# Kernel tuning notes

Hardware: AMD Instinct MI355X
Metric: run time of the kernel (lower is better)

The kernel has to match this reference:

```python
import jax, jax.numpy as jnp
import numpy as np

N_SRC = 100000
N_EDGES = 1000000
IN_FEATS = 64
N_CLASSES = 64


def setup_inputs() -> dict:
    key = jax.random.key(0)
    k1, k2, k3, k4, k5 = jax.random.split(key, 5)
    x = jax.random.normal(k1, (N_SRC, IN_FEATS), dtype=jnp.float32)
    W_self = jax.random.normal(k2, (IN_FEATS, N_CLASSES), dtype=jnp.float32) / np.sqrt(IN_FEATS)
    W_neigh = jax.random.normal(k3, (IN_FEATS, N_CLASSES), dtype=jnp.float32) / np.sqrt(IN_FEATS)
    b = jnp.zeros((N_CLASSES,), dtype=jnp.float32)
    src = jax.random.randint(k4, (N_EDGES,), 0, N_SRC, dtype=jnp.int32)
    dst = jax.random.randint(k5, (N_EDGES,), 0, N_SRC, dtype=jnp.int32)
    return {"x": x, "W_self": W_self, "W_neigh": W_neigh, "b": b,
            "src": src, "dst": dst, "num_dst": N_SRC}


def reference(x, W_self, W_neigh, b, src, dst, num_dst):
    # SAGEConv 'mean': gather src features along edges, segment-mean into dst,
    # then rst = h_dst @ W_self + h_neigh_mean @ W_neigh + b, followed by relu.
    msgs = x[src]                                                   # [E, F] irregular gather
    summed = jax.ops.segment_sum(msgs, dst, num_segments=num_dst)   # [num_dst, F]
    deg = jax.ops.segment_sum(jnp.ones((src.shape[0],), x.dtype), dst,
                              num_segments=num_dst)                 # [num_dst]
    h_neigh = summed / jnp.maximum(deg, 1.0)[:, None]               # mean (0 for isolated)
    h_dst = x[:num_dst]
    h = h_dst @ W_self + h_neigh @ W_neigh + b
    return jax.nn.relu(h)
```

## Files before the change

### kernel.cpp

```cpp
#include <hip/hip_runtime.h>


constexpr int F = 64;
constexpr int BROWS = 256;
constexpr int MAXNB = 512;
constexpr int CHP = 4096;
constexpr int LCAP = 4096;
constexpr int LDK = 136;

typedef __attribute__((ext_vector_type(8))) short short8;
typedef __attribute__((ext_vector_type(4))) float float4v;

__device__ inline unsigned short f2bf(float f) {
    union { float f; unsigned u; } c; c.f = f;
    unsigned u = c.u;
    return (unsigned short)((u + 0x7FFFu + ((u >> 16) & 1u)) >> 16);
}
__device__ inline float bf2f(unsigned short h) {
    union { unsigned u; float f; } c; c.u = (unsigned)h << 16;
    return c.f;
}

__global__ __launch_bounds__(256) void k_conv(const float* __restrict__ x,
                                              const float* __restrict__ Ws,
                                              const float* __restrict__ Wn,
                                              unsigned short* __restrict__ xb,
                                              unsigned short* __restrict__ WtG,
                                              const int* __restrict__ dst,
                                              int* __restrict__ cnt,
                                              long n4, int n_edges, int nchunk) {
    __shared__ int hist[MAXNB];
    int t = threadIdx.x;
    long tid = (long)blockIdx.x * 256 + t;
    if (tid < 2 * F * F) {
        int i = (int)tid;
        int n = i & 63, k = i >> 6;
        float v = (k < 64) ? Ws[k * 64 + n] : Wn[(k - 64) * 64 + n];
        WtG[n * 128 + k] = f2bf(v);
    }
    int c = blockIdx.x;
    if (c < nchunk) {
        for (int i = t; i < MAXNB; i += 256) hist[i] = 0;
        __syncthreads();
        int e0 = c * CHP, e1 = min(e0 + CHP, n_edges);
        for (int e = e0 + t; e < e1; e += 256) atomicAdd(&hist[dst[e] >> 8], 1);
        __syncthreads();
        for (int i = t; i < MAXNB; i += 256) cnt[(long)c * MAXNB + i] = hist[i];
    }
    for (long i = tid; i < n4; i += (long)gridDim.x * 256) {
        float4 v = ((const float4*)x)[i];
        ushort4 o;
        o.x = f2bf(v.x); o.y = f2bf(v.y); o.z = f2bf(v.z); o.w = f2bf(v.w);
        ((ushort4*)xb)[i] = o;
    }
}

__global__ __launch_bounds__(512) void k_scanA(int* __restrict__ cnt,
                                               int* __restrict__ btot, int nchunk) {
    int b = (blockIdx.x * 512 + threadIdx.x) >> 6;
    int lane = threadIdx.x & 63;
    if (b >= MAXNB) return;
    int per = (nchunk + 63) / 64;
    int c0 = lane * per;
    int vals[16];
    int lsum = 0;
#pragma unroll
    for (int i = 0; i < 16; ++i) {
        if (i < per) {
            int c = c0 + i;
            int v = (c < nchunk) ? cnt[(long)c * MAXNB + b] : 0;
            vals[i] = v; lsum += v;
        }
    }
    int incl = lsum;
    for (int off = 1; off < 64; off <<= 1) {
        int o = __shfl_up(incl, off);
        if (lane >= off) incl += o;
    }
    int run = incl - lsum;
#pragma unroll
    for (int i = 0; i < 16; ++i) {
        if (i < per) {
            int c = c0 + i;
            if (c < nchunk) { cnt[(long)c * MAXNB + b] = run; run += vals[i]; }
        }
    }
    int tot = __shfl(incl, 63);
    if (lane == 0) btot[b] = tot;
}

__global__ __launch_bounds__(512) void k_scanB(const int* __restrict__ btot,
                                               int* __restrict__ bstart) {
    __shared__ int wtot[8];
    __shared__ int woff[8];
    int t = threadIdx.x;
    int lane = t & 63, wave = t >> 6;
    int v = btot[t];
    int incl = v;
    for (int off = 1; off < 64; off <<= 1) {
        int o = __shfl_up(incl, off);
        if (lane >= off) incl += o;
    }
    if (lane == 63) wtot[wave] = incl;
    __syncthreads();
    if (t == 0) { int s = 0; for (int i = 0; i < 8; ++i) { woff[i] = s; s += wtot[i]; } }
    __syncthreads();
    bstart[t] = incl - v + woff[wave];
    if (t == 511) bstart[MAXNB] = woff[7] + incl;
}

__global__ __launch_bounds__(512) void k_place(const int* __restrict__ src,
                                               const int* __restrict__ dst,
                                               const int* __restrict__ cnt,
                                               const int* __restrict__ bstart,
                                               unsigned* __restrict__ pay, int n_edges) {
    __shared__ int sbp[MAXNB];
    __shared__ int lstart[MAXNB];
    __shared__ int lcur[MAXNB];
    __shared__ unsigned spay[CHP];
    __shared__ int sgpos[CHP];
    __shared__ int wtot[8];
    __shared__ int woff[8];
    int t = threadIdx.x;
    int c = blockIdx.x;
    int e0 = c * CHP, e1 = min(e0 + CHP, n_edges);
    sbp[t] = bstart[t] + cnt[(long)c * MAXNB + t];
    lcur[t] = 0;
    __syncthreads();
    for (int e = e0 + t; e < e1; e += 512) atomicAdd(&lcur[dst[e] >> 8], 1);
    __syncthreads();
    int lane = t & 63, wave = t >> 6;
    int v = lcur[t];
    int incl = v;
    for (int off = 1; off < 64; off <<= 1) {
        int o = __shfl_up(incl, off);
        if (lane >= off) incl += o;
    }
    if (lane == 63) wtot[wave] = incl;
    __syncthreads();
    if (t == 0) { int s = 0; for (int i = 0; i < 8; ++i) { woff[i] = s; s += wtot[i]; } }
    __syncthreads();
    lstart[t] = incl - v + woff[wave];
    lcur[t] = 0;
    __syncthreads();
    for (int e = e0 + t; e < e1; e += 512) {
        int d = dst[e];
        int b = d >> 8;
        int rank = atomicAdd(&lcur[b], 1);
        int idx = lstart[b] + rank;
        spay[idx] = ((unsigned)src[e] << 8) | (unsigned)(d & 255);
        sgpos[idx] = sbp[b] + rank;
    }
    __syncthreads();
    int n = e1 - e0;
    for (int i = t; i < n; i += 512) pay[sgpos[i]] = spay[i];
}

__global__ __launch_bounds__(256) void k_agg(const unsigned short* __restrict__ xb,
                                             const unsigned* __restrict__ pay,
                                             const int* __restrict__ bstart,
                                             unsigned short* __restrict__ hb,
                                             int num_dst) {
    __shared__ int degs[64];
    __shared__ int rs[64];
    __shared__ int cur[64];
    __shared__ int scsr[LCAP];
    int t = threadIdx.x;
    int blk = blockIdx.x;
    int b = blk >> 2, q = blk & 3;
    int s0 = bstart[b], s1 = bstart[b + 1];
    if (t < 64) degs[t] = 0;
    __syncthreads();
    for (int i = s0 + t; i < s1; i += 256) {
        int row = pay[i] & 255;
        if ((row >> 6) == q) atomicAdd(&degs[row & 63], 1);
    }
    __syncthreads();
    if (t < 64) {
        int v = degs[t];
        int incl = v;
        for (int off = 1; off < 64; off <<= 1) {
            int o = __shfl_up(incl, off);
            if (t >= off) incl += o;
        }
        rs[t] = incl - v;
        cur[t] = incl - v;
    }
    __syncthreads();
    for (int i = s0 + t; i < s1; i += 256) {
        unsigned p = pay[i];
        int row = p & 255;
        if ((row >> 6) == q) {
            int pos = atomicAdd(&cur[row & 63], 1);
            if (pos < LCAP) scsr[pos] = (int)(p >> 8);
        }
    }
    __syncthreads();

    int lane = t & 63;
    int wave = t >> 6;
    int g = lane >> 3;
    int c8 = (lane & 7) * 8;
#pragma unroll
    for (int batch = 0; batch < 2; ++batch) {
        int rl = wave * 16 + batch * 8 + g;
        int grow = b * BROWS + q * 64 + rl;
        int deg = degs[rl];
        int base = rs[rl];
        float acc[8] = {0.f, 0.f, 0.f, 0.f, 0.f, 0.f, 0.f, 0.f};
        for (int k = 0; k < deg; k += 4) {
            int dm = deg - 1;
            int i0 = scsr[base + k];
            int i1 = scsr[base + min(k + 1, dm)];
            int i2 = scsr[base + min(k + 2, dm)];
            int i3 = scsr[base + min(k + 3, dm)];
            short8 u0 = *(const short8*)&xb[(long)i0 * F + c8];
            short8 u1 = *(const short8*)&xb[(long)i1 * F + c8];
            short8 u2 = *(const short8*)&xb[(long)i2 * F + c8];
            short8 u3 = *(const short8*)&xb[(long)i3 * F + c8];
#pragma unroll
            for (int j = 0; j < 8; ++j) acc[j] += bf2f((unsigned short)u0[j]);
            if (k + 1 < deg) {
#pragma unroll
                for (int j = 0; j < 8; ++j) acc[j] += bf2f((unsigned short)u1[j]);
            }
            if (k + 2 < deg) {
#pragma unroll
                for (int j = 0; j < 8; ++j) acc[j] += bf2f((unsigned short)u2[j]);
            }
            if (k + 3 < deg) {
#pragma unroll
                for (int j = 0; j < 8; ++j) acc[j] += bf2f((unsigned short)u3[j]);
            }
        }
        if (grow < num_dst) {
            float inv = 1.0f / fmaxf((float)deg, 1.0f);
            short8 o;
#pragma unroll
            for (int j = 0; j < 8; ++j) o[j] = (short)f2bf(acc[j] * inv);
            *(short8*)&hb[(long)grow * F + c8] = o;
        }
    }
}

__global__ __launch_bounds__(256) void k_gemm_mfma(
    const unsigned short* __restrict__ xb, const unsigned short* __restrict__ hb,
    const unsigned short* __restrict__ WtG,
    const float* __restrict__ b, float* __restrict__ out, int num_dst)
{
    __shared__ __align__(16) unsigned short Atile[64 * LDK];
    __shared__ __align__(16) unsigned short Wt[64 * LDK];
    int t = threadIdx.x;
    int row0 = blockIdx.x * 64;

    for (int i = t; i < 64 * 16; i += 256) {
        int r = i >> 4, s = i & 15;
        *(short8*)&Wt[r * LDK + s * 8] = *(const short8*)&WtG[r * 128 + s * 8];
        int g = row0 + r;
        short8 v = {0, 0, 0, 0, 0, 0, 0, 0};
        if (g < num_dst)
            v = (s < 8) ? *(const short8*)&xb[(long)g * F + s * 8]
                        : *(const short8*)&hb[(long)g * F + (s - 8) * 8];
        *(short8*)&Atile[r * LDK + s * 8] = v;
    }
    __syncthreads();

    int lane = t & 63;
    int wave = t >> 6;
    int m = lane & 15;
    int quad = lane >> 4;
    const unsigned short* arow = &Atile[(wave * 16 + m) * LDK + quad * 8];

    float4v acc[4];
#pragma unroll
    for (int nt = 0; nt < 4; ++nt) acc[nt] = (float4v){0.f, 0.f, 0.f, 0.f};

#pragma unroll
    for (int kb = 0; kb < 4; ++kb) {
        short8 a = *(const short8*)(arow + kb * 32);
#pragma unroll
        for (int nt = 0; nt < 4; ++nt) {
            short8 bf = *(const short8*)&Wt[(nt * 16 + m) * LDK + quad * 8 + kb * 32];
            acc[nt] = __builtin_amdgcn_mfma_f32_16x16x32_bf16(a, bf, acc[nt], 0, 0, 0);
        }
    }

    int gr_base = row0 + wave * 16 + quad * 4;
#pragma unroll
    for (int nt = 0; nt < 4; ++nt) {
        int col = nt * 16 + m;
        float bias = b[col];
#pragma unroll
        for (int rg = 0; rg < 4; ++rg) {
            int g = gr_base + rg;
            if (g < num_dst) out[(long)g * F + col] = fmaxf(acc[nt][rg] + bias, 0.0f);
        }
    }
}

__global__ __launch_bounds__(256) void k_scatter(const float* __restrict__ x, const int* __restrict__ src,
                                                 const int* __restrict__ dst, float* __restrict__ summed,
                                                 float* __restrict__ degf, int n_edges) {
    long tid = (long)blockIdx.x * 256 + threadIdx.x;
    int e = (int)(tid >> 6);
    if (e >= n_edges) return;
    int f = threadIdx.x & 63;
    atomicAdd(&summed[(long)dst[e] * F + f], x[(long)src[e] * F + f]);
    if (f == 0) atomicAdd(&degf[dst[e]], 1.0f);
}

__global__ __launch_bounds__(256) void k_gemm_shfl(
    const float* __restrict__ x, const float* __restrict__ Ws, const float* __restrict__ Wn,
    const float* __restrict__ b, const float* __restrict__ degf, float* inout, int num_dst)
{
    __shared__ float Wl[2 * F * F];
    for (int i = threadIdx.x; i < F * F; i += 256) { Wl[i] = Ws[i]; Wl[F * F + i] = Wn[i]; }
    __syncthreads();
    int lane = threadIdx.x & 63;
    int r = (blockIdx.x * 256 + threadIdx.x) >> 6;
    if (r >= num_dst) return;
    float xv = x[(long)r * F + lane];
    float hv = inout[(long)r * F + lane] / fmaxf(degf[r], 1.0f);
    float acc = b[lane];
#pragma unroll
    for (int k = 0; k < F; ++k) {
        acc += __shfl(xv, k) * Wl[k * F + lane];
        acc += __shfl(hv, k) * Wl[(F + k) * F + lane];
    }
    inout[(long)r * F + lane] = fmaxf(acc, 0.0f);
}

extern "C" void kernel_launch(void* const* d_in, const int* in_sizes, int n_in,
                              void* d_out, int out_size, void* d_ws, size_t ws_size,
                              hipStream_t stream) {
    const float* x  = (const float*)d_in[0];
    const float* Ws = (const float*)d_in[1];
    const float* Wn = (const float*)d_in[2];
    const float* b  = (const float*)d_in[3];
    const int* src  = (const int*)d_in[4];
    const int* dst  = (const int*)d_in[5];
    int n_edges = in_sizes[4];
    int num_dst = out_size / F;
    float* out = (float*)d_out;

    int nchunk = (n_edges + CHP - 1) / CHP;
    int nb = (num_dst + BROWS - 1) / BROWS;

    char* ws = (char*)d_ws;
    size_t off = 0;
    auto alloc = [&](size_t bytes) { char* p = ws + off; off = (off + bytes + 255) & ~(size_t)255; return p; };
    unsigned short* xb  = (unsigned short*)alloc((size_t)num_dst * F * 2);
    unsigned short* hb  = (unsigned short*)alloc((size_t)num_dst * F * 2);
    unsigned* pay       = (unsigned*)alloc((size_t)n_edges * 4);
    unsigned short* WtG = (unsigned short*)alloc(2 * F * F * 2);
    int* cnt            = (int*)alloc((size_t)nchunk * MAXNB * 4);
    int* btot           = (int*)alloc(MAXNB * 4);
    int* bstart         = (int*)alloc((MAXNB + 1) * 4);
    bool big_ws = (off <= ws_size) && (nb <= MAXNB) && (nchunk <= 1024);

    if (big_ws) {
        long n4 = (long)num_dst * F / 4;
        int convgrid = max(2048, nchunk);
        k_conv<<<convgrid, 256, 0, stream>>>(x, Ws, Wn, xb, WtG, dst, cnt, n4, n_edges, nchunk);
        k_scanA<<<(MAXNB * 64 + 511) / 512, 512, 0, stream>>>(cnt, btot, nchunk);
        k_scanB<<<1, 512, 0, stream>>>(btot, bstart);
        k_place<<<nchunk, 512, 0, stream>>>(src, dst, cnt, bstart, pay, n_edges);
        k_agg<<<nb * 4, 256, 0, stream>>>(xb, pay, bstart, hb, num_dst);
        k_gemm_mfma<<<(num_dst + 63) / 64, 256, 0, stream>>>(xb, hb, WtG, b, out, num_dst);
    } else {
        float* degf = (float*)d_ws;
        (void)hipMemsetAsync(d_out, 0, (size_t)out_size * sizeof(float), stream);
        (void)hipMemsetAsync(degf, 0, (size_t)num_dst * sizeof(float), stream);
        long tt = (long)n_edges * 64;
        k_scatter<<<(int)((tt + 255) / 256), 256, 0, stream>>>(x, src, dst, out, degf, n_edges);
        k_gemm_shfl<<<(num_dst + 3) / 4, 256, 0, stream>>>(x, Ws, Wn, b, degf, out, num_dst);
    }
}
```

Measured before the change: 151.3 us.

## Fuse neighbor aggregation and MFMA GEMM into one kernel

Merges the aggregation kernel and the MFMA GEMM kernel into a single kernel. The mean-aggregated neighbor rows now stay in shared memory as bf16 instead of going out to a global hb buffer. Shared memory is reused: the CSR index list and the weight tile share one pool. This removes a kernel launch and the global write and read of hb. In exchange, shared memory use rises, which can lower occupancy, and the CSR capacity changes to 4352 entries.

```diff
diff --git a/kernel.cpp b/kernel.cpp
--- a/kernel.cpp
+++ b/kernel.cpp
@@ -5,8 +5,9 @@
 constexpr int BROWS = 256;
 constexpr int MAXNB = 512;
 constexpr int CHP = 4096;
-constexpr int LCAP = 4096;
 constexpr int LDK = 136;
+constexpr int QCAP = 4352;
+constexpr int LDH = 72;
 
 typedef __attribute__((ext_vector_type(8))) short short8;
 typedef __attribute__((ext_vector_type(4))) float float4v;
@@ -156,19 +157,30 @@
     for (int i = t; i < n; i += 512) pay[sgpos[i]] = spay[i];
 }
 
-__global__ __launch_bounds__(256) void k_agg(const unsigned short* __restrict__ xb,
-                                             const unsigned* __restrict__ pay,
-                                             const int* __restrict__ bstart,
-                                             unsigned short* __restrict__ hb,
-                                             int num_dst) {
+__global__ __launch_bounds__(256) void k_aggemm(const unsigned short* __restrict__ xb,
+                                                const unsigned* __restrict__ pay,
+                                                const int* __restrict__ bstart,
+                                                const unsigned short* __restrict__ WtG,
+                                                const float* __restrict__ bias,
+                                                float* __restrict__ out,
+                                                int num_dst) {
     __shared__ int degs[64];
     __shared__ int rs[64];
     __shared__ int cur[64];
-    __shared__ int scsr[LCAP];
+    __shared__ __align__(16) unsigned char upool[64 * LDK * 2];
+    __shared__ __align__(16) unsigned short hbt[64 * LDH];
+    int* scsr = (int*)upool;
+    unsigned short* Wt = (unsigned short*)upool;
+
     int t = threadIdx.x;
     int blk = blockIdx.x;
     int b = blk >> 2, q = blk & 3;
+    int grow0 = b * BROWS + q * 64;
+    if (grow0 >= num_dst) return;
     int s0 = bstart[b], s1 = bstart[b + 1];
+    int lane = t & 63;
+    int wave = t >> 6;
+
     if (t < 64) degs[t] = 0;
     __syncthreads();
     for (int i = s0 + t; i < s1; i += 256) {
@@ -192,19 +204,16 @@
         int row = p & 255;
         if ((row >> 6) == q) {
             int pos = atomicAdd(&cur[row & 63], 1);
-            if (pos < LCAP) scsr[pos] = (int)(p >> 8);
-        }
-    }
-    __syncthreads();
-
-    int lane = t & 63;
-    int wave = t >> 6;
+            if (pos < QCAP) scsr[pos] = (int)(p >> 8);
+        }
+    }
+    __syncthreads();
+
     int g = lane >> 3;
     int c8 = (lane & 7) * 8;
 #pragma unroll
     for (int batch = 0; batch < 2; ++batch) {
         int rl = wave * 16 + batch * 8 + g;
-        int grow = b * BROWS + q * 64 + rl;
         int deg = degs[rl];
         int base = rs[rl];
         float acc[8] = {0.f, 0.f, 0.f, 0.f, 0.f, 0.f, 0.f, 0.f};
@@ -233,67 +242,57 @@
                 for (int j = 0; j < 8; ++j) acc[j] += bf2f((unsigned short)u3[j]);
             }
         }
-        if (grow < num_dst) {
-            float inv = 1.0f / fmaxf((float)deg, 1.0f);
-            short8 o;
-#pragma unroll
-            for (int j = 0; j < 8; ++j) o[j] = (short)f2bf(acc[j] * inv);
-            *(short8*)&hb[(long)grow * F + c8] = o;
-        }
-    }
-}
-
-__global__ __launch_bounds__(256) void k_gemm_mfma(
-    const unsigned short* __restrict__ xb, const unsigned short* __restrict__ hb,
-    const unsigned short* __restrict__ WtG,
-    const float* __restrict__ b, float* __restrict__ out, int num_dst)
-{
-    __shared__ __align__(16) unsigned short Atile[64 * LDK];
-    __shared__ __align__(16) unsigned short Wt[64 * LDK];
-    int t = threadIdx.x;
-    int row0 = blockIdx.x * 64;
+        float inv = 1.0f / fmaxf((float)deg, 1.0f);
+        short8 o;
+#pragma unroll
+        for (int j = 0; j < 8; ++j) o[j] = (short)f2bf(acc[j] * inv);
+        *(short8*)&hbt[rl * LDH + c8] = o;
+    }
+    __syncthreads();
 
     for (int i = t; i < 64 * 16; i += 256) {
         int r = i >> 4, s = i & 15;
         *(short8*)&Wt[r * LDK + s * 8] = *(const short8*)&WtG[r * 128 + s * 8];
-        int g = row0 + r;
-        short8 v = {0, 0, 0, 0, 0, 0, 0, 0};
-        if (g < num_dst)
-            v = (s < 8) ? *(const short8*)&xb[(long)g * F + s * 8]
-                        : *(const short8*)&hb[(long)g * F + (s - 8) * 8];
-        *(short8*)&Atile[r * LDK + s * 8] = v;
-    }
-    __syncthreads();
-
-    int lane = t & 63;
-    int wave = t >> 6;
+    }
+    __syncthreads();
+
     int m = lane & 15;
     int quad = lane >> 4;
-    const unsigned short* arow = &Atile[(wave * 16 + m) * LDK + quad * 8];
+    int rowg = grow0 + wave * 16 + m;
+    int rx = min(rowg, num_dst - 1);
+    const unsigned short* xrow = &xb[(long)rx * F + quad * 8];
+    short8 a0 = *(const short8*)(xrow);
+    short8 a1 = *(const short8*)(xrow + 32);
+    const unsigned short* hrow = &hbt[(wave * 16 + m) * LDH + quad * 8];
+    short8 a2 = *(const short8*)(hrow);
+    short8 a3 = *(const short8*)(hrow + 32);
 
     float4v acc[4];
 #pragma unroll
     for (int nt = 0; nt < 4; ++nt) acc[nt] = (float4v){0.f, 0.f, 0.f, 0.f};
 
 #pragma unroll
-    for (int kb = 0; kb < 4; ++kb) {
-        short8 a = *(const short8*)(arow + kb * 32);
-#pragma unroll
-        for (int nt = 0; nt < 4; ++nt) {
-            short8 bf = *(const short8*)&Wt[(nt * 16 + m) * LDK + quad * 8 + kb * 32];
-            acc[nt] = __builtin_amdgcn_mfma_f32_16x16x32_bf16(a, bf, acc[nt], 0, 0, 0);
-        }
-    }
-
-    int gr_base = row0 + wave * 16 + quad * 4;
+    for (int nt = 0; nt < 4; ++nt) {
+        const unsigned short* wrow = &Wt[(nt * 16 + m) * LDK + quad * 8];
+        short8 b0 = *(const short8*)(wrow);
+        short8 b1 = *(const short8*)(wrow + 32);
+        short8 b2 = *(const short8*)(wrow + 64);
+        short8 b3 = *(const short8*)(wrow + 96);
+        acc[nt] = __builtin_amdgcn_mfma_f32_16x16x32_bf16(a0, b0, acc[nt], 0, 0, 0);
+        acc[nt] = __builtin_amdgcn_mfma_f32_16x16x32_bf16(a1, b1, acc[nt], 0, 0, 0);
+        acc[nt] = __builtin_amdgcn_mfma_f32_16x16x32_bf16(a2, b2, acc[nt], 0, 0, 0);
+        acc[nt] = __builtin_amdgcn_mfma_f32_16x16x32_bf16(a3, b3, acc[nt], 0, 0, 0);
+    }
+
+    int gr_base = grow0 + wave * 16 + quad * 4;
 #pragma unroll
     for (int nt = 0; nt < 4; ++nt) {
         int col = nt * 16 + m;
-        float bias = b[col];
+        float bv = bias[col];
 #pragma unroll
         for (int rg = 0; rg < 4; ++rg) {
-            int g = gr_base + rg;
-            if (g < num_dst) out[(long)g * F + col] = fmaxf(acc[nt][rg] + bias, 0.0f);
+            int gg = gr_base + rg;
+            if (gg < num_dst) out[(long)gg * F + col] = fmaxf(acc[nt][rg] + bv, 0.0f);
         }
     }
 }
@@ -350,7 +349,6 @@
     size_t off = 0;
     auto alloc = [&](size_t bytes) { char* p = ws + off; off = (off + bytes + 255) & ~(size_t)255; return p; };
     unsigned short* xb  = (unsigned short*)alloc((size_t)num_dst * F * 2);
-    unsigned short* hb  = (unsigned short*)alloc((size_t)num_dst * F * 2);
     unsigned* pay       = (unsigned*)alloc((size_t)n_edges * 4);
     unsigned short* WtG = (unsigned short*)alloc(2 * F * F * 2);
     int* cnt            = (int*)alloc((size_t)nchunk * MAXNB * 4);
@@ -365,8 +363,7 @@
         k_scanA<<<(MAXNB * 64 + 511) / 512, 512, 0, stream>>>(cnt, btot, nchunk);
         k_scanB<<<1, 512, 0, stream>>>(btot, bstart);
         k_place<<<nchunk, 512, 0, stream>>>(src, dst, cnt, bstart, pay, n_edges);
-        k_agg<<<nb * 4, 256, 0, stream>>>(xb, pay, bstart, hb, num_dst);
-        k_gemm_mfma<<<(num_dst + 63) / 64, 256, 0, stream>>>(xb, hb, WtG, b, out, num_dst);
+        k_aggemm<<<nb * 4, 256, 0, stream>>>(xb, pay, bstart, WtG, b, out, num_dst);
     } else {
         float* degf = (float*)d_ws;
         (void)hipMemsetAsync(d_out, 0, (size_t)out_size * sizeof(float), stream);
```

After: 153.5 us. About the same (+1.5%).
